# Kernel optimization log

Measured on AMD Instinct MI355X. Metric: run time of the kernel, lower is better.

The kernel has to match this reference:

```python
import jax, jax.numpy as jnp
import numpy as np

B, D, H, O, E = 65536, 128, 256, 8, 8  # batch, input_dim, hidden_dim, output_dim, n_phases


def setup_inputs() -> dict:
    key = jax.random.key(0)
    ks = jax.random.split(key, 6)
    scale = 0.05
    x = jax.random.normal(ks[0], (B, D), dtype=jnp.float32)
    phases = jax.random.randint(ks[1], (B,), 0, E, dtype=jnp.int32)
    Ws = jax.random.normal(ks[2], (D, H), dtype=jnp.float32) * scale  # shared Linear weight (transposed)
    bs = jnp.zeros((H,), dtype=jnp.float32)
    W1 = jax.random.normal(ks[3], (E, H, H), dtype=jnp.float32) * scale  # per-head first Linear
    b1 = jnp.zeros((E, H), dtype=jnp.float32)
    W2 = jax.random.normal(ks[4], (E, H, O), dtype=jnp.float32) * scale  # per-head second Linear
    b2 = jnp.zeros((E, O), dtype=jnp.float32)
    return {"x": x, "phases": phases, "Ws": Ws, "bs": bs,
            "W1": W1, "b1": b1, "W2": W2, "b2": b2}


def reference(x, phases, Ws, bs, W1, b1, W2, b2):
    # shared trunk: Linear + ReLU
    h = jax.nn.relu(x @ Ws + bs)                                # [B, H]
    # run every head on every sample (dense grouped GEMM), then gather the
    # per-sample routed head. NOTE: no activation between the two head Linears,
    # matching nn.Sequential(Linear, Linear) in the source.
    h1 = jnp.einsum('bh,ehk->ebk', h, W1) + b1[:, None, :]      # [E, B, H]
    y = jnp.einsum('ebk,eko->ebo', h1, W2) + b2[:, None, :]     # [E, B, O]
    q = y[phases, jnp.arange(x.shape[0])]                       # [B, O] routed select
    return q
```

## Files before the change

kernel.cpp:

```cpp
#include <hip/hip_runtime.h>
#include <hip/hip_bf16.h>
#include <cstdint>


using bf16x8 = __attribute__((ext_vector_type(8))) __bf16;
using f32x4  = __attribute__((ext_vector_type(4))) float;

__device__ __forceinline__ unsigned short bf16b(float f) {
    __bf16 h = (__bf16)f;
    return __builtin_bit_cast(unsigned short, h);
}
__device__ __forceinline__ unsigned pack2(float a, float b) {
    return (unsigned)bf16b(a) | ((unsigned)bf16b(b) << 16);
}

__global__ void prep_kernel(const float* __restrict__ Ws,
                            const float* __restrict__ b1,
                            const float* __restrict__ W1,
                            const float* __restrict__ W2,
                            const float* __restrict__ b2,
                            unsigned short* __restrict__ wsT,
                            unsigned short* __restrict__ wfT,
                            float* __restrict__ bfuse) {
    const int bid = blockIdx.x, tid = threadIdx.x;
    if (bid < 64) {
        __shared__ float w2s[2048];
        const int e = bid >> 3, part = bid & 7;
        const float* W2e = W2 + (size_t)e * 2048;
        {
            float4* dst = (float4*)w2s;
            const float4* src = (const float4*)W2e;
            dst[tid]       = src[tid];
            dst[256 + tid] = src[256 + tid];
        }
        __syncthreads();
        const int mloc = tid >> 3, g = tid & 7;
        const int m = part * 32 + mloc;
        const float* w1row = W1 + ((size_t)e * 256 + m) * 256;
        float acc[8] = {0,0,0,0,0,0,0,0};
        #pragma unroll
        for (int i = 0; i < 32; ++i) {
            int k = g + i * 8;
            float a = w1row[k];
            const float* w2r = w2s + k * 8;
            #pragma unroll
            for (int o = 0; o < 8; ++o) acc[o] += a * w2r[o];
        }
        #pragma unroll
        for (int o = 0; o < 8; ++o) {
            acc[o] += __shfl_xor(acc[o], 1);
            acc[o] += __shfl_xor(acc[o], 2);
            acc[o] += __shfl_xor(acc[o], 4);
        }
        if (g == 0) {
            #pragma unroll
            for (int o = 0; o < 8; ++o)
                wfT[(size_t)(e * 8 + o) * 256 + m] = bf16b(acc[o]);
        }
    } else if (bid < 68) {
        #pragma unroll
        for (int it = 0; it < 8; ++it) {
            int c = (bid - 64) * 2048 + it * 256 + tid;
            int k = c >> 6, n0 = (c & 63) * 4;
            float4 v = *(const float4*)(Ws + (size_t)k * 256 + n0);
            wsT[(n0 + 0) * 128 + k] = bf16b(v.x);
            wsT[(n0 + 1) * 128 + k] = bf16b(v.y);
            wsT[(n0 + 2) * 128 + k] = bf16b(v.z);
            wsT[(n0 + 3) * 128 + k] = bf16b(v.w);
        }
    } else {
        const int e = tid >> 5, l = tid & 31;
        float acc[8] = {0,0,0,0,0,0,0,0};
        #pragma unroll
        for (int i = 0; i < 8; ++i) {
            int k = l * 8 + i;
            float a = b1[e * 256 + k];
            const float* w2r = W2 + ((size_t)(e * 256 + k)) * 8;
            #pragma unroll
            for (int o = 0; o < 8; ++o) acc[o] += a * w2r[o];
        }
        #pragma unroll
        for (int o = 0; o < 8; ++o) {
            acc[o] += __shfl_xor(acc[o], 1);
            acc[o] += __shfl_xor(acc[o], 2);
            acc[o] += __shfl_xor(acc[o], 4);
            acc[o] += __shfl_xor(acc[o], 8);
            acc[o] += __shfl_xor(acc[o], 16);
        }
        if (l == 0) {
            #pragma unroll
            for (int o = 0; o < 8; ++o)
                bfuse[e * 8 + o] = acc[o] + b2[e * 8 + o];
        }
    }
}

#define T_TILES 2

__global__ __launch_bounds__(256, 2) void fused_kernel(
    const float* __restrict__ x,
    const int* __restrict__ phases,
    const float* __restrict__ bs,
    const bf16x8* __restrict__ wsA_g,
    const bf16x8* __restrict__ wfB_g,
    const float* __restrict__ bfuse,
    float* __restrict__ out) {
    __shared__ __align__(16) char lds[16384 + 32768 + 512];
    char* xs = lds;
    char* hs = lds + 16384;
    int* ph_s = (int*)(lds + 49152);

    const int tid = threadIdx.x;
    const int lane = tid & 63;
    const int wv = tid >> 6;
    const int l15 = lane & 15;
    const int lhi = lane >> 4;

    bf16x8 wsA[4][4];
    #pragma unroll
    for (int hi = 0; hi < 4; ++hi) {
        int n = wv * 64 + hi * 16 + l15;
        #pragma unroll
        for (int kg = 0; kg < 4; ++kg)
            wsA[hi][kg] = wsA_g[n * 16 + kg * 4 + lhi];
    }
    bf16x8 wfB[8];
    {
        int c = wv * 16 + l15;
        #pragma unroll
        for (int kg = 0; kg < 8; ++kg)
            wfB[kg] = wfB_g[c * 32 + kg * 4 + lhi];
    }
    f32x4 bsv[4];
    #pragma unroll
    for (int hi = 0; hi < 4; ++hi)
        bsv[hi] = *(const f32x4*)(bs + wv * 64 + hi * 16 + lhi * 4);
    const float bfv = bfuse[wv * 16 + l15];
    const int myE = wv * 2 + (l15 >> 3);
    const int co  = l15 & 7;

    const float4* xg = (const float4*)x;

    {
        int row0 = (blockIdx.x * T_TILES) * 64;
        #pragma unroll
        for (int it = 0; it < 4; ++it) {
            int c = it * 256 + tid;
            int row = c >> 4, col8 = c & 15;
            int gi = (row0 + row) * 32 + col8 * 2;
            float4 a = xg[gi], d = xg[gi + 1];
            uint4 u;
            u.x = pack2(a.x, a.y); u.y = pack2(a.z, a.w);
            u.z = pack2(d.x, d.y); u.w = pack2(d.z, d.w);
            unsigned addr = (unsigned)(row * 256 + col8 * 16);
            addr ^= (unsigned)((row & 7) << 4);
            *(uint4*)(xs + addr) = u;
        }
        if (tid < 64) ph_s[tid] = phases[row0 + tid];
    }

    for (int t = 0; t < T_TILES; ++t) {
        const int row0 = (blockIdx.x * T_TILES + t) * 64;
        __syncthreads();

        f32x4 acc1[4][4];
        #pragma unroll
        for (int hi = 0; hi < 4; ++hi)
            #pragma unroll
            for (int bi = 0; bi < 4; ++bi)
                acc1[hi][bi] = bsv[hi];
        #pragma unroll
        for (int kg = 0; kg < 4; ++kg) {
            bf16x8 xb[4];
            #pragma unroll
            for (int bi = 0; bi < 4; ++bi) {
                int b = bi * 16 + l15;
                unsigned addr = (unsigned)(b * 256 + (kg * 32 + lhi * 8) * 2);
                addr ^= (unsigned)((b & 7) << 4);
                xb[bi] = *(const bf16x8*)(xs + addr);
            }
            #pragma unroll
            for (int hi = 0; hi < 4; ++hi)
                #pragma unroll
                for (int bi = 0; bi < 4; ++bi)
                    acc1[hi][bi] = __builtin_amdgcn_mfma_f32_16x16x32_bf16(
                        wsA[hi][kg], xb[bi], acc1[hi][bi], 0, 0, 0);
        }
        #pragma unroll
        for (int hi = 0; hi < 4; ++hi)
            #pragma unroll
            for (int bi = 0; bi < 4; ++bi) {
                float v0 = acc1[hi][bi][0]; v0 = v0 > 0.f ? v0 : 0.f;
                float v1 = acc1[hi][bi][1]; v1 = v1 > 0.f ? v1 : 0.f;
                float v2 = acc1[hi][bi][2]; v2 = v2 > 0.f ? v2 : 0.f;
                float v3 = acc1[hi][bi][3]; v3 = v3 > 0.f ? v3 : 0.f;
                uint2 u; u.x = pack2(v0, v1); u.y = pack2(v2, v3);
                int b = bi * 16 + l15;
                int n0 = wv * 64 + hi * 16 + lhi * 4;
                unsigned addr = (unsigned)(b * 512 + n0 * 2);
                addr ^= (unsigned)((b & 7) << 4);
                *(uint2*)(hs + addr) = u;
            }
        __syncthreads();

        f32x4 acc2[4];
        #pragma unroll
        for (int mi = 0; mi < 4; ++mi)
            acc2[mi] = (f32x4){bfv, bfv, bfv, bfv};
        #pragma unroll
        for (int kg = 0; kg < 8; ++kg) {
            bf16x8 ha[4];
            #pragma unroll
            for (int mi = 0; mi < 4; ++mi) {
                int b = mi * 16 + l15;
                unsigned addr = (unsigned)(b * 512 + (kg * 32 + lhi * 8) * 2);
                addr ^= (unsigned)((b & 7) << 4);
                ha[mi] = *(const bf16x8*)(hs + addr);
            }
            #pragma unroll
            for (int mi = 0; mi < 4; ++mi)
                acc2[mi] = __builtin_amdgcn_mfma_f32_16x16x32_bf16(
                    ha[mi], wfB[kg], acc2[mi], 0, 0, 0);
        }
        #pragma unroll
        for (int mi = 0; mi < 4; ++mi)
            #pragma unroll
            for (int r = 0; r < 4; ++r) {
                int b = mi * 16 + lhi * 4 + r;
                int e = ph_s[(t & 1) * 64 + b];
                if (e == myE)
                    out[(size_t)(row0 + b) * 8 + co] = acc2[mi][r];
            }

        if (t + 1 < T_TILES) {
            int nrow0 = row0 + 64;
            #pragma unroll
            for (int it = 0; it < 4; ++it) {
                int c = it * 256 + tid;
                int row = c >> 4, col8 = c & 15;
                int gi = (nrow0 + row) * 32 + col8 * 2;
                float4 a = xg[gi], d = xg[gi + 1];
                uint4 u;
                u.x = pack2(a.x, a.y); u.y = pack2(a.z, a.w);
                u.z = pack2(d.x, d.y); u.w = pack2(d.z, d.w);
                unsigned addr = (unsigned)(row * 256 + col8 * 16);
                addr ^= (unsigned)((row & 7) << 4);
                *(uint4*)(xs + addr) = u;
            }
            if (tid < 64) ph_s[((t + 1) & 1) * 64 + tid] = phases[nrow0 + tid];
        }
    }
}

extern "C" void kernel_launch(void* const* d_in, const int* in_sizes, int n_in,
                              void* d_out, int out_size, void* d_ws, size_t ws_size,
                              hipStream_t stream) {
    const float* x      = (const float*)d_in[0];
    const int*   phases = (const int*)d_in[1];
    const float* Ws     = (const float*)d_in[2];
    const float* bs     = (const float*)d_in[3];
    const float* W1     = (const float*)d_in[4];
    const float* b1     = (const float*)d_in[5];
    const float* W2     = (const float*)d_in[6];
    const float* b2     = (const float*)d_in[7];
    float* out = (float*)d_out;

    unsigned short* wsT   = (unsigned short*)d_ws;
    unsigned short* wfT   = (unsigned short*)((char*)d_ws + 65536);
    float*          bfuse = (float*)((char*)d_ws + 98304);

    prep_kernel<<<69, 256, 0, stream>>>(Ws, b1, W1, W2, b2, wsT, wfT, bfuse);
    fused_kernel<<<512, 256, 0, stream>>>(
        x, phases, bs, (const bf16x8*)wsT, (const bf16x8*)wfT, bfuse, out);
}
```

Baseline: 26.34 us.

## Parallelize weight prep across more blocks and load both x tiles upfront

The prep kernel now splits the W1·W2 fold across 256 blocks with a transposed W2 in LDS, and transposes Ws using coalesced reads with packed 16-byte stores, across 16 blocks. The fused kernel issues global loads for both 64-row x tiles at once into separate LDS buffers, replacing the serialized load-compute-load sequence. It also reads phases straight from global memory instead of staging them in LDS. This is meant to cut prep-kernel latency and expose more memory parallelism, at the cost of 64KB LDS per block, which may limit occupancy to one block per CU.

```diff
diff --git a/kernel.cpp b/kernel.cpp
--- a/kernel.cpp
+++ b/kernel.cpp
@@ -23,61 +23,35 @@
                             unsigned short* __restrict__ wfT,
                             float* __restrict__ bfuse) {
     const int bid = blockIdx.x, tid = threadIdx.x;
-    if (bid < 64) {
-        __shared__ float w2s[2048];
-        const int e = bid >> 3, part = bid & 7;
+    if (bid < 256) {
+        __shared__ float w2sT[8][256];
+        const int e = bid >> 5, mc = bid & 31;
         const float* W2e = W2 + (size_t)e * 2048;
         {
-            float4* dst = (float4*)w2s;
-            const float4* src = (const float4*)W2e;
-            dst[tid]       = src[tid];
-            dst[256 + tid] = src[256 + tid];
+            #pragma unroll
+            for (int h = 0; h < 2; ++h) {
+                int f4 = h * 256 + tid;
+                float4 v = ((const float4*)W2e)[f4];
+                int k = f4 >> 1, o4 = (f4 & 1) * 4;
+                w2sT[o4 + 0][k] = v.x;
+                w2sT[o4 + 1][k] = v.y;
+                w2sT[o4 + 2][k] = v.z;
+                w2sT[o4 + 3][k] = v.w;
+            }
         }
         __syncthreads();
-        const int mloc = tid >> 3, g = tid & 7;
-        const int m = part * 32 + mloc;
+        const int mloc = tid >> 5, kg = tid & 31;
+        const int m = mc * 8 + mloc;
         const float* w1row = W1 + ((size_t)e * 256 + m) * 256;
+        float w1v[8];
+        #pragma unroll
+        for (int i = 0; i < 8; ++i) w1v[i] = w1row[kg + i * 32];
         float acc[8] = {0,0,0,0,0,0,0,0};
         #pragma unroll
-        for (int i = 0; i < 32; ++i) {
-            int k = g + i * 8;
-            float a = w1row[k];
-            const float* w2r = w2s + k * 8;
-            #pragma unroll
-            for (int o = 0; o < 8; ++o) acc[o] += a * w2r[o];
-        }
-        #pragma unroll
-        for (int o = 0; o < 8; ++o) {
-            acc[o] += __shfl_xor(acc[o], 1);
-            acc[o] += __shfl_xor(acc[o], 2);
-            acc[o] += __shfl_xor(acc[o], 4);
-        }
-        if (g == 0) {
-            #pragma unroll
-            for (int o = 0; o < 8; ++o)
-                wfT[(size_t)(e * 8 + o) * 256 + m] = bf16b(acc[o]);
-        }
-    } else if (bid < 68) {
-        #pragma unroll
-        for (int it = 0; it < 8; ++it) {
-            int c = (bid - 64) * 2048 + it * 256 + tid;
-            int k = c >> 6, n0 = (c & 63) * 4;
-            float4 v = *(const float4*)(Ws + (size_t)k * 256 + n0);
-            wsT[(n0 + 0) * 128 + k] = bf16b(v.x);
-            wsT[(n0 + 1) * 128 + k] = bf16b(v.y);
-            wsT[(n0 + 2) * 128 + k] = bf16b(v.z);
-            wsT[(n0 + 3) * 128 + k] = bf16b(v.w);
-        }
-    } else {
-        const int e = tid >> 5, l = tid & 31;
-        float acc[8] = {0,0,0,0,0,0,0,0};
-        #pragma unroll
         for (int i = 0; i < 8; ++i) {
-            int k = l * 8 + i;
-            float a = b1[e * 256 + k];
-            const float* w2r = W2 + ((size_t)(e * 256 + k)) * 8;
-            #pragma unroll
-            for (int o = 0; o < 8; ++o) acc[o] += a * w2r[o];
+            int k = kg + i * 32;
+            #pragma unroll
+            for (int o = 0; o < 8; ++o) acc[o] += w1v[i] * w2sT[o][k];
         }
         #pragma unroll
         for (int o = 0; o < 8; ++o) {
@@ -87,6 +61,41 @@
             acc[o] += __shfl_xor(acc[o], 8);
             acc[o] += __shfl_xor(acc[o], 16);
         }
+        if (kg == 0) {
+            #pragma unroll
+            for (int o = 0; o < 8; ++o)
+                wfT[(size_t)(e * 8 + o) * 256 + m] = bf16b(acc[o]);
+        }
+    } else if (bid < 272) {
+        const int kgb = bid - 256;
+        const int n = tid;
+        float w[8];
+        #pragma unroll
+        for (int j = 0; j < 8; ++j)
+            w[j] = Ws[(size_t)(kgb * 8 + j) * 256 + n];
+        uint4 u;
+        u.x = pack2(w[0], w[1]); u.y = pack2(w[2], w[3]);
+        u.z = pack2(w[4], w[5]); u.w = pack2(w[6], w[7]);
+        *(uint4*)(wsT + (size_t)n * 128 + kgb * 8) = u;
+    } else {
+        const int e = tid >> 5, l = tid & 31;
+        float acc[8] = {0,0,0,0,0,0,0,0};
+        #pragma unroll
+        for (int i = 0; i < 8; ++i) {
+            int k = l * 8 + i;
+            float a = b1[e * 256 + k];
+            const float* w2r = W2 + ((size_t)(e * 256 + k)) * 8;
+            #pragma unroll
+            for (int o = 0; o < 8; ++o) acc[o] += a * w2r[o];
+        }
+        #pragma unroll
+        for (int o = 0; o < 8; ++o) {
+            acc[o] += __shfl_xor(acc[o], 1);
+            acc[o] += __shfl_xor(acc[o], 2);
+            acc[o] += __shfl_xor(acc[o], 4);
+            acc[o] += __shfl_xor(acc[o], 8);
+            acc[o] += __shfl_xor(acc[o], 16);
+        }
         if (l == 0) {
             #pragma unroll
             for (int o = 0; o < 8; ++o)
@@ -94,8 +103,6 @@
         }
     }
 }
-
-#define T_TILES 2
 
 __global__ __launch_bounds__(256, 2) void fused_kernel(
     const float* __restrict__ x,
@@ -105,16 +112,17 @@
     const bf16x8* __restrict__ wfB_g,
     const float* __restrict__ bfuse,
     float* __restrict__ out) {
-    __shared__ __align__(16) char lds[16384 + 32768 + 512];
-    char* xs = lds;
-    char* hs = lds + 16384;
-    int* ph_s = (int*)(lds + 49152);
+    __shared__ __align__(16) char lds[65536];
+    char* xs0 = lds;
+    char* xs1 = lds + 16384;
+    char* hs  = lds + 32768;
 
     const int tid = threadIdx.x;
     const int lane = tid & 63;
     const int wv = tid >> 6;
     const int l15 = lane & 15;
     const int lhi = lane >> 4;
+    const int blk0 = blockIdx.x * 128;
 
     bf16x8 wsA[4][4];
     #pragma unroll
@@ -140,28 +148,37 @@
     const int co  = l15 & 7;
 
     const float4* xg = (const float4*)x;
-
-    {
-        int row0 = (blockIdx.x * T_TILES) * 64;
-        #pragma unroll
-        for (int it = 0; it < 4; ++it) {
-            int c = it * 256 + tid;
-            int row = c >> 4, col8 = c & 15;
-            int gi = (row0 + row) * 32 + col8 * 2;
-            float4 a = xg[gi], d = xg[gi + 1];
-            uint4 u;
-            u.x = pack2(a.x, a.y); u.y = pack2(a.z, a.w);
-            u.z = pack2(d.x, d.y); u.w = pack2(d.z, d.w);
-            unsigned addr = (unsigned)(row * 256 + col8 * 16);
-            addr ^= (unsigned)((row & 7) << 4);
-            *(uint4*)(xs + addr) = u;
-        }
-        if (tid < 64) ph_s[tid] = phases[row0 + tid];
-    }
-
-    for (int t = 0; t < T_TILES; ++t) {
-        const int row0 = (blockIdx.x * T_TILES + t) * 64;
-        __syncthreads();
+    float4 a0[4], d0[4], a1[4], d1[4];
+    #pragma unroll
+    for (int it = 0; it < 4; ++it) {
+        int c = it * 256 + tid;
+        int row = c >> 4, col8 = c & 15;
+        int gi0 = (blk0 + row) * 32 + col8 * 2;
+        a0[it] = xg[gi0]; d0[it] = xg[gi0 + 1];
+        int gi1 = (blk0 + 64 + row) * 32 + col8 * 2;
+        a1[it] = xg[gi1]; d1[it] = xg[gi1 + 1];
+    }
+    #pragma unroll
+    for (int it = 0; it < 4; ++it) {
+        int c = it * 256 + tid;
+        int row = c >> 4, col8 = c & 15;
+        unsigned addr = (unsigned)(row * 256 + col8 * 16);
+        addr ^= (unsigned)((row & 7) << 4);
+        uint4 u;
+        u.x = pack2(a0[it].x, a0[it].y); u.y = pack2(a0[it].z, a0[it].w);
+        u.z = pack2(d0[it].x, d0[it].y); u.w = pack2(d0[it].z, d0[it].w);
+        *(uint4*)(xs0 + addr) = u;
+        uint4 v;
+        v.x = pack2(a1[it].x, a1[it].y); v.y = pack2(a1[it].z, a1[it].w);
+        v.z = pack2(d1[it].x, d1[it].y); v.w = pack2(d1[it].z, d1[it].w);
+        *(uint4*)(xs1 + addr) = v;
+    }
+    __syncthreads();
+
+    #pragma unroll
+    for (int t = 0; t < 2; ++t) {
+        const char* xs = t ? xs1 : xs0;
+        const int row0 = blk0 + t * 64;
 
         f32x4 acc1[4][4];
         #pragma unroll
@@ -227,28 +244,11 @@
             #pragma unroll
             for (int r = 0; r < 4; ++r) {
                 int b = mi * 16 + lhi * 4 + r;
-                int e = ph_s[(t & 1) * 64 + b];
+                int e = phases[row0 + b];
                 if (e == myE)
                     out[(size_t)(row0 + b) * 8 + co] = acc2[mi][r];
             }
-
-        if (t + 1 < T_TILES) {
-            int nrow0 = row0 + 64;
-            #pragma unroll
-            for (int it = 0; it < 4; ++it) {
-                int c = it * 256 + tid;
-                int row = c >> 4, col8 = c & 15;
-                int gi = (nrow0 + row) * 32 + col8 * 2;
-                float4 a = xg[gi], d = xg[gi + 1];
-                uint4 u;
-                u.x = pack2(a.x, a.y); u.y = pack2(a.z, a.w);
-                u.z = pack2(d.x, d.y); u.w = pack2(d.z, d.w);
-                unsigned addr = (unsigned)(row * 256 + col8 * 16);
-                addr ^= (unsigned)((row & 7) << 4);
-                *(uint4*)(xs + addr) = u;
-            }
-            if (tid < 64) ph_s[((t + 1) & 1) * 64 + tid] = phases[nrow0 + tid];
-        }
+        if (t == 0) __syncthreads();
     }
 }
 
@@ -269,7 +269,7 @@
     unsigned short* wfT   = (unsigned short*)((char*)d_ws + 65536);
     float*          bfuse = (float*)((char*)d_ws + 98304);
 
-    prep_kernel<<<69, 256, 0, stream>>>(Ws, b1, W1, W2, b2, wsT, wfT, bfuse);
+    prep_kernel<<<273, 256, 0, stream>>>(Ws, b1, W1, W2, b2, wsT, wfT, bfuse);
     fused_kernel<<<512, 256, 0, stream>>>(
         x, phases, bs, (const bf16x8*)wsT, (const bf16x8*)wfT, bfuse, out);
 }
```

Result: slower. 30.07 us (+14.2%).
